# Optimization experiments

Hardware: AMD Instinct MI355X
Metric: run time of the kernel (lower is better)

## Reference

```python
import jax, jax.numpy as jnp
import numpy as np

EPS = 1e-5
N_HEADS = 16
D_NOPE = 128
D_ROPE = 64
D_QK = D_NOPE + D_ROPE  # 192
D_V = 128
KV_RANK = 512
SCALE = D_QK ** -0.5


def rms_norm(x, w, eps=EPS):
    return x * jax.lax.rsqrt(jnp.mean(x * x, axis=-1, keepdims=True) + eps) * w


def apply_rope(x, c, s):
    # x: [..., D_ROPE], c/s broadcastable [..., D_ROPE//2]; half-split rotation
    x0, x1 = x[..., : D_ROPE // 2], x[..., D_ROPE // 2 :]
    return jnp.concatenate([x0 * c - x1 * s, x0 * s + x1 * c], axis=-1)


def setup_inputs() -> dict:
    key = jax.random.key(0)
    ks = jax.random.split(key, 8)
    B, S, H_DIM = 2, 2048, 2048
    Q_RANK = 1536
    w = lambda k, shp: jax.random.normal(k, shp, dtype=jnp.float32) * 0.02
    # real RoPE tables: [max_seq, D_ROPE//2]
    inv_freq = 1.0 / (10000.0 ** (np.arange(0, D_ROPE, 2, dtype=np.float32) / D_ROPE))
    ang = np.arange(S, dtype=np.float32)[:, None] * inv_freq[None, :]
    return {
        "x": jax.random.normal(ks[0], (B, S, H_DIM), dtype=jnp.float32),
        "positions": jnp.arange(S, dtype=jnp.int64),
        "Wqa": w(ks[1], (H_DIM, Q_RANK)),
        "g_qa": jnp.ones((Q_RANK,), jnp.float32),
        "Wqb": w(ks[2], (Q_RANK, N_HEADS * D_QK)),
        "Wkva": w(ks[3], (H_DIM, KV_RANK + D_ROPE)),
        "g_kva": jnp.ones((KV_RANK,), jnp.float32),
        "Wkvb": w(ks[4], (KV_RANK, N_HEADS * (D_NOPE + D_V))),
        "Wo": w(ks[5], (N_HEADS * D_V, H_DIM)),
        "cos": jnp.asarray(np.cos(ang)),
        "sin": jnp.asarray(np.sin(ang)),
    }


def reference(x, positions, Wqa, g_qa, Wqb, Wkva, g_kva, Wkvb, Wo, cos, sin):
    B, S, _ = x.shape
    # Q path: low-rank down, RMSNorm, up
    q = rms_norm(x @ Wqa, g_qa) @ Wqb  # [B,S,H*D_QK]
    q = q.reshape(B, S, N_HEADS, D_QK)
    q_nope, q_rope = q[..., :D_NOPE], q[..., D_NOPE:]
    c = cos[positions]  # [S, D_ROPE//2]
    s = sin[positions]
    q_rope = apply_rope(q_rope, c[None, :, None, :], s[None, :, None, :])
    # KV path: joint down-proj, split latent / rope-key
    kv_a = x @ Wkva  # [B,S,KV_RANK+D_ROPE]
    kv_latent = rms_norm(kv_a[..., :KV_RANK], g_kva)
    k_rope = apply_rope(kv_a[..., KV_RANK:], c[None, :, :], s[None, :, :])  # [B,S,D_ROPE]
    # up-project latent to per-head k_nope and v
    kv_b = (kv_latent @ Wkvb).reshape(B, S, N_HEADS, D_NOPE + D_V)
    k_nope, v = kv_b[..., :D_NOPE], kv_b[..., D_NOPE:]
    k = jnp.concatenate(
        [k_nope, jnp.broadcast_to(k_rope[:, :, None, :], (B, S, N_HEADS, D_ROPE))], axis=-1
    )  # [B,S,H,D_QK]
    q_full = jnp.concatenate([q_nope, q_rope], axis=-1)  # [B,S,H,D_QK]
    # causal SDPA with d_qk != d_v
    scores = jnp.einsum("bqhd,bkhd->bhqk", q_full, k) * SCALE
    causal = jnp.tril(jnp.ones((S, S), dtype=bool))
    scores = jnp.where(causal[None, None, :, :], scores, -jnp.inf)
    p = jax.nn.softmax(scores, axis=-1)
    out = jnp.einsum("bhqk,bkhd->bqhd", p, v).reshape(B, S, N_HEADS * D_V)
    return out @ Wo
```

## Files before the change

kernel.cpp:

```cpp
#include <hip/hip_runtime.h>
#include <hip/hip_bf16.h>

typedef __bf16 bf16;
typedef __bf16 bf16x8 __attribute__((ext_vector_type(8)));
typedef __bf16 bf16x4 __attribute__((ext_vector_type(4)));
typedef float f32x4 __attribute__((ext_vector_type(4)));

#define B_    2
#define S_    2048
#define HD    2048
#define NH    16
#define DQK   192
#define DV    128
#define QR    1536
#define KVR   512
#define NTOK  4096
#define NKVB  4096
#define NQB   3072
#define NQKVA 2176

#define EXP2F(x) __builtin_amdgcn_exp2f(x)

static __device__ __forceinline__ void gload16(const void* g, void* l) {
  __builtin_amdgcn_global_load_lds(
      (const __attribute__((address_space(1))) void*)g,
      (__attribute__((address_space(3))) void*)l, 16, 0, 0);
}

__global__ __launch_bounds__(256) void cvt_bf16(const float* __restrict__ in,
                                                bf16* __restrict__ out, long n) {
  long i = ((long)blockIdx.x * 256 + threadIdx.x) * 4;
  if (i + 3 < n) {
    float4 v = *(const float4*)(in + i);
    bf16x4 o = {(bf16)v.x, (bf16)v.y, (bf16)v.z, (bf16)v.w};
    *(bf16x4*)(out + i) = o;
  }
}

__global__ __launch_bounds__(256) void transpose_cvt(const float* __restrict__ in,
                                                     bf16* __restrict__ out,
                                                     int R, int C, int Np) {
  __shared__ float tile[32][33];
  int c0 = blockIdx.x * 32;
  int r0 = blockIdx.y * 32;
  int tx = threadIdx.x & 31, ty = threadIdx.x >> 5;
#pragma unroll
  for (int i = 0; i < 4; ++i) {
    int r = r0 + ty + i * 8, c = c0 + tx;
    tile[ty + i * 8][tx] = (c < C) ? in[(long)r * C + c] : 0.f;
  }
  __syncthreads();
#pragma unroll
  for (int i = 0; i < 4; ++i) {
    int oc = c0 + ty + i * 8;
    if (oc < Np) out[(long)oc * R + r0 + tx] = (bf16)tile[tx][ty + i * 8];
  }
}

#define GEMM_CORE(A, Bt, K)                                                    \
  __shared__ bf16 As[128 * 64];                                                \
  __shared__ bf16 Bs[128 * 64];                                                \
  const int t = threadIdx.x;                                                   \
  const int l = t & 63;                                                        \
  const int w = t >> 6;                                                        \
  const int m0 = blockIdx.y * 128;                                             \
  const int n0 = blockIdx.x * 128;                                             \
  const int wr = (w >> 1) * 64;                                                \
  const int wc = (w & 1) * 64;                                                 \
  const int lr = l & 15;                                                       \
  const int lg = l >> 4;                                                       \
  f32x4 acc[4][4] = {};                                                        \
  for (int k0 = 0; k0 < (K); k0 += 64) {                                       \
    __syncthreads();                                                           \
    _Pragma("unroll")                                                          \
    for (int j = 0; j < 4; ++j) {                                              \
      int s = j * 256 + t;                                                     \
      int row = s >> 3, sc = s & 7;                                            \
      int c = sc ^ (row & 7);                                                  \
      gload16((A) + (long)(m0 + row) * (K) + k0 + c * 8,                       \
              As + (j * 256 + w * 64) * 8);                                    \
      gload16((Bt) + (long)(n0 + row) * (K) + k0 + c * 8,                      \
              Bs + (j * 256 + w * 64) * 8);                                    \
    }                                                                          \
    __syncthreads();                                                           \
    _Pragma("unroll")                                                          \
    for (int kh = 0; kh < 2; ++kh) {                                           \
      bf16x8 af[4], bfr[4];                                                    \
      _Pragma("unroll")                                                        \
      for (int m = 0; m < 4; ++m) {                                            \
        int row = wr + m * 16 + lr;                                            \
        af[m] = *(const bf16x8*)(As + row * 64 + (((kh * 4 + lg) ^ (row & 7)) << 3)); \
      }                                                                        \
      _Pragma("unroll")                                                        \
      for (int n = 0; n < 4; ++n) {                                            \
        int row = wc + n * 16 + lr;                                            \
        bfr[n] = *(const bf16x8*)(Bs + row * 64 + (((kh * 4 + lg) ^ (row & 7)) << 3)); \
      }                                                                        \
      _Pragma("unroll")                                                        \
      for (int m = 0; m < 4; ++m)                                              \
        _Pragma("unroll")                                                      \
        for (int n = 0; n < 4; ++n)                                            \
          acc[m][n] = __builtin_amdgcn_mfma_f32_16x16x32_bf16(af[m], bfr[n], acc[m][n], 0, 0, 0); \
    }                                                                          \
  }

template <typename CT>
__global__ __launch_bounds__(256) void gemm_bf16(const bf16* __restrict__ A,
                                                 const bf16* __restrict__ Bt,
                                                 CT* __restrict__ C,
                                                 int M, int N, int K) {
  GEMM_CORE(A, Bt, K)
#pragma unroll
  for (int m = 0; m < 4; ++m)
#pragma unroll
    for (int n = 0; n < 4; ++n)
#pragma unroll
      for (int v = 0; v < 4; ++v) {
        int row = m0 + wr + m * 16 + lg * 4 + v;
        int col = n0 + wc + n * 16 + lr;
        C[(long)row * N + col] = (CT)acc[m][n][v];
      }
}

__global__ __launch_bounds__(256) void gemm_qf(const bf16* __restrict__ A,
                                               const bf16* __restrict__ Bt,
                                               const int* __restrict__ pos,
                                               const float* __restrict__ cosT,
                                               const float* __restrict__ sinT,
                                               bf16* __restrict__ q_bhsd) {
  const float SCALE = 0.07216878364870323f * 1.4426950408889634f;
  GEMM_CORE(A, Bt, QR)
  int c0 = n0 + wc;
  int h = c0 / 192;
  int part = c0 - h * 192;
#pragma unroll
  for (int m = 0; m < 4; ++m)
#pragma unroll
    for (int v = 0; v < 4; ++v) {
      int row = m0 + wr + m * 16 + lg * 4 + v;
      int b = row >> 11, s = row & (S_ - 1);
      long base = ((long)(b * NH + h) * S_ + s) * DQK;
      if (part < 128) {
#pragma unroll
        for (int n = 0; n < 4; ++n)
          q_bhsd[base + part + n * 16 + lr] = (bf16)(acc[m][n][v] * SCALE);
      } else {
        int p = pos[s] & (S_ - 1);
        float c_lo = cosT[p * 32 + lr],      s_lo = sinT[p * 32 + lr];
        float c_hi = cosT[p * 32 + 16 + lr], s_hi = sinT[p * 32 + 16 + lr];
        float o0 = acc[m][0][v] * c_lo - acc[m][2][v] * s_lo;
        float o1 = acc[m][1][v] * c_hi - acc[m][3][v] * s_hi;
        float o2 = acc[m][0][v] * s_lo + acc[m][2][v] * c_lo;
        float o3 = acc[m][1][v] * s_hi + acc[m][3][v] * c_hi;
        q_bhsd[base + 128 + lr] = (bf16)(o0 * SCALE);
        q_bhsd[base + 144 + lr] = (bf16)(o1 * SCALE);
        q_bhsd[base + 160 + lr] = (bf16)(o2 * SCALE);
        q_bhsd[base + 176 + lr] = (bf16)(o3 * SCALE);
      }
    }
}

__global__ __launch_bounds__(256) void gemm_kvb(const bf16* __restrict__ A,
                                                const bf16* __restrict__ Bt,
                                                bf16* __restrict__ k_bhsd,
                                                bf16* __restrict__ v_rows) {
  GEMM_CORE(A, Bt, KVR)
  int c0 = n0 + wc;
  int h = c0 >> 8;
  int dbase = c0 & 64;
  bool vpart = (c0 >> 7) & 1;
#pragma unroll
  for (int m = 0; m < 4; ++m)
#pragma unroll
    for (int v = 0; v < 4; ++v) {
      int row = m0 + wr + m * 16 + lg * 4 + v;
      int b = row >> 11, s = row & (S_ - 1);
      if (!vpart) {
        long base = ((long)(b * NH + h) * S_ + s) * DQK + dbase;
#pragma unroll
        for (int n = 0; n < 4; ++n)
          k_bhsd[base + n * 16 + lr] = (bf16)acc[m][n][v];
      } else {
        long base = (long)row * 2048 + h * 128 + dbase;
#pragma unroll
        for (int n = 0; n < 4; ++n)
          v_rows[base + n * 16 + lr] = (bf16)acc[m][n][v];
      }
    }
}

__global__ __launch_bounds__(256) void norm_prep(const bf16* __restrict__ xa,
                                                 const float* __restrict__ g_qa,
                                                 const float* __restrict__ g_kva,
                                                 const int* __restrict__ pos,
                                                 const float* __restrict__ cosT,
                                                 const float* __restrict__ sinT,
                                                 bf16* __restrict__ q_n,
                                                 bf16* __restrict__ kv_l,
                                                 bf16* __restrict__ k_bhsd) {
  int row = blockIdx.x;
  int t = threadIdx.x;
  int b = row >> 11, s = row & (S_ - 1);
  const bf16* xr = xa + (long)row * NQKVA;
  __shared__ float red[3];
  __shared__ bf16 rope_s[64];
  float vf[8];
  if (t < 192) {
    bf16x8 vv = *(const bf16x8*)(xr + t * 8);
    float ss = 0.f;
#pragma unroll
    for (int e = 0; e < 8; ++e) { vf[e] = (float)vv[e]; ss += vf[e] * vf[e]; }
#pragma unroll
    for (int m = 1; m < 64; m <<= 1) ss += __shfl_xor(ss, m);
    if ((t & 63) == 0) red[t >> 6] = ss;
  } else {
    int tt = t - 192;
    const bf16* xl = xr + QR;
    bf16x8 vv = *(const bf16x8*)(xl + tt * 8);
    float ss = 0.f;
#pragma unroll
    for (int e = 0; e < 8; ++e) { vf[e] = (float)vv[e]; ss += vf[e] * vf[e]; }
#pragma unroll
    for (int m = 1; m < 64; m <<= 1) ss += __shfl_xor(ss, m);
    float rs = rsqrtf(ss / KVR + 1e-5f);
    bf16x8 o;
#pragma unroll
    for (int e = 0; e < 8; ++e) o[e] = (bf16)(vf[e] * rs * g_kva[tt * 8 + e]);
    *(bf16x8*)(kv_l + (long)row * KVR + tt * 8) = o;
    if (tt < 32) {
      int p = pos[s] & (S_ - 1);
      float c = cosT[p * 32 + tt], sn = sinT[p * 32 + tt];
      float x0 = (float)xl[512 + tt], x1 = (float)xl[544 + tt];
      rope_s[tt] = (bf16)(x0 * c - x1 * sn);
      rope_s[32 + tt] = (bf16)(x0 * sn + x1 * c);
    }
  }
  __syncthreads();
  if (t < 192) {
    float ss = red[0] + red[1] + red[2];
    float rs = rsqrtf(ss / QR + 1e-5f);
    bf16x8 o;
#pragma unroll
    for (int e = 0; e < 8; ++e) o[e] = (bf16)(vf[e] * rs * g_qa[t * 8 + e]);
    *(bf16x8*)(q_n + (long)row * QR + t * 8) = o;
  } else {
    int tt = t - 192;
    bf16x8 rv = *(const bf16x8*)&rope_s[(tt & 7) * 8];
    long base0 = ((long)(b * NH + (tt >> 3)) * S_ + s) * DQK + 128 + (tt & 7) * 8;
    long base1 = ((long)(b * NH + 8 + (tt >> 3)) * S_ + s) * DQK + 128 + (tt & 7) * 8;
    *(bf16x8*)(k_bhsd + base0) = rv;
    *(bf16x8*)(k_bhsd + base1) = rv;
  }
}

__global__ __launch_bounds__(256) void v_trans(const bf16* __restrict__ v_rows,
                                               bf16* __restrict__ v_t) {
  __shared__ bf16 tile[32][33];
  int st = blockIdx.x, dt = blockIdx.y, bh = blockIdx.z;
  int b = bh >> 4, h = bh & 15;
  int tx = threadIdx.x & 31, ty = threadIdx.x >> 5;
#pragma unroll
  for (int i = 0; i < 4; ++i) {
    int s = st * 32 + ty + i * 8, d = dt * 32 + tx;
    tile[ty + i * 8][tx] = v_rows[((long)(b * S_ + s)) * 2048 + h * 128 + d];
  }
  __syncthreads();
#pragma unroll
  for (int i = 0; i < 4; ++i) {
    int d = dt * 32 + ty + i * 8, s = st * 32 + tx;
    v_t[((long)bh * DV + d) * S_ + s] = tile[tx][ty + i * 8];
  }
}

#define QBLK 64
#define KVB  64
#define DVP  144
__global__ __launch_bounds__(256) void flash2(const bf16* __restrict__ q_bhsd,
                                              const bf16* __restrict__ k_bhsd,
                                              const bf16* __restrict__ v_t,
                                              bf16* __restrict__ att) {
  __shared__ bf16 Ks[KVB * DQK];
  __shared__ bf16 Vs[DVP * KVB];
  __shared__ bf16 Ps[4][16 * 72];
  int bid = blockIdx.x;
  int bh = bid & 31;
  int qt = 31 - (bid >> 5);
  int b = bh >> 4, h = bh & 15;
  int q0 = qt * QBLK;
  int t = threadIdx.x;
  int w = t >> 6, l = t & 63;
  int lr = l & 15, lg = l >> 4;
  int qw = q0 + w * 16;

  const bf16* Qb = q_bhsd + (long)bh * S_ * DQK;
  const bf16* Kb = k_bhsd + (long)bh * S_ * DQK;
  const bf16* Vb = v_t + (long)bh * DV * S_;

  if (t < 128) {
    int rr = 128 + (t >> 3), cc = (t & 7) * 8;
    bf16 val = (bf16)((rr == 128) ? 1.0f : 0.0f);
    bf16x8 vvv = {val, val, val, val, val, val, val, val};
    *(bf16x8*)(Vs + rr * KVB + cc) = vvv;
  }

  bf16x8 qf[6];
#pragma unroll
  for (int t6 = 0; t6 < 6; ++t6)
    qf[t6] = *(const bf16x8*)(Qb + (long)(qw + lr) * DQK + t6 * 32 + lg * 8);

  f32x4 oacc[9] = {};
  float mrow[4] = {-1e30f, -1e30f, -1e30f, -1e30f};
  const int lr7 = lr & 7;

  int nkt = qt + 1;
  for (int kt = 0; kt < nkt; ++kt) {
    int k0 = kt * KVB;
    __syncthreads();
#pragma unroll
    for (int j = 0; j < 6; ++j) {
      int s = j * 256 + t;
      int r = s / 24, c1 = s - r * 24;
      int c = c1 ^ (r & 7);
      gload16(Kb + (long)(k0 + r) * DQK + c * 8, Ks + (j * 256 + w * 64) * 8);
    }
#pragma unroll
    for (int j = 0; j < 4; ++j) {
      int s = j * 256 + t;
      int d = s >> 3, c1 = s & 7;
      int c = c1 ^ (d & 7);
      gload16(Vb + (long)d * S_ + k0 + c * 8, Vs + (j * 256 + w * 64) * 8);
    }
    __syncthreads();
    if (k0 > qw + 15) continue;

    f32x4 sacc[4] = {};
#pragma unroll
    for (int n = 0; n < 4; ++n) {
      int rk = n * 16 + lr;
#pragma unroll
      for (int t6 = 0; t6 < 6; ++t6) {
        bf16x8 kf = *(const bf16x8*)(Ks + rk * DQK + (((t6 * 4 + lg) ^ lr7) << 3));
        sacc[n] = __builtin_amdgcn_mfma_f32_16x16x32_bf16(qf[t6], kf, sacc[n], 0, 0, 0);
      }
    }
    if (k0 + KVB - 1 > qw) {
#pragma unroll
      for (int n = 0; n < 4; ++n)
#pragma unroll
        for (int v = 0; v < 4; ++v) {
          int r = lg * 4 + v, c = n * 16 + lr;
          if (k0 + c > qw + r) sacc[n][v] = -1e30f;
        }
    }
    float corr[4], p[4][4];
#pragma unroll
    for (int v = 0; v < 4; ++v) {
      float mv = fmaxf(fmaxf(sacc[0][v], sacc[1][v]), fmaxf(sacc[2][v], sacc[3][v]));
#pragma unroll
      for (int msk = 1; msk < 16; msk <<= 1) mv = fmaxf(mv, __shfl_xor(mv, msk));
      float mt = fmaxf(mrow[v], mv);
      corr[v] = EXP2F(mrow[v] - mt);
#pragma unroll
      for (int n = 0; n < 4; ++n) p[n][v] = EXP2F(sacc[n][v] - mt);
      mrow[v] = mt;
    }
#pragma unroll
    for (int dn = 0; dn < 9; ++dn)
#pragma unroll
      for (int v = 0; v < 4; ++v) oacc[dn][v] *= corr[v];
#pragma unroll
    for (int v = 0; v < 4; ++v)
#pragma unroll
      for (int n = 0; n < 4; ++n)
        Ps[w][(lg * 4 + v) * 72 + n * 16 + lr] = (bf16)p[n][v];
#pragma unroll
    for (int kc = 0; kc < 2; ++kc) {
      bf16x8 pf = *(const bf16x8*)(Ps[w] + lr * 72 + kc * 32 + lg * 8);
#pragma unroll
      for (int dn = 0; dn < 9; ++dn) {
        int d = dn * 16 + lr;
        bf16x8 vf = *(const bf16x8*)(Vs + d * KVB + (((kc * 4 + lg) ^ lr7) << 3));
        oacc[dn] = __builtin_amdgcn_mfma_f32_16x16x32_bf16(pf, vf, oacc[dn], 0, 0, 0);
      }
    }
  }
  float rl[4];
#pragma unroll
  for (int v = 0; v < 4; ++v) {
    float lv = __shfl(oacc[8][v], lg * 16);
    rl[v] = 1.0f / lv;
  }
#pragma unroll
  for (int dn = 0; dn < 8; ++dn)
#pragma unroll
    for (int v = 0; v < 4; ++v) {
      int r = lg * 4 + v;
      float o = oacc[dn][v] * rl[v];
      att[((long)(b * S_ + qw + r)) * 2048 + h * 128 + dn * 16 + lr] = (bf16)o;
    }
}

extern "C" void kernel_launch(void* const* d_in, const int* in_sizes, int n_in,
                              void* d_out, int out_size, void* d_ws, size_t ws_size,
                              hipStream_t stream) {
  const float* x        = (const float*)d_in[0];
  const int* pos        = (const int*)d_in[1];
  const float* Wqa      = (const float*)d_in[2];
  const float* g_qa     = (const float*)d_in[3];
  const float* Wqb      = (const float*)d_in[4];
  const float* Wkva     = (const float*)d_in[5];
  const float* g_kva    = (const float*)d_in[6];
  const float* Wkvb     = (const float*)d_in[7];
  const float* Wo       = (const float*)d_in[8];
  const float* cosT     = (const float*)d_in[9];
  const float* sinT     = (const float*)d_in[10];
  float* out            = (float*)d_out;

  size_t off = 0;
  char* wsp = (char*)d_ws;
  auto alloc = [&](size_t n) { void* p = wsp + off; off += (n + 255) & ~(size_t)255; return p; };
  bf16*  Wqa_t  = (bf16*) alloc((size_t)QR * HD * 2);
  bf16*  Wkva_t = (bf16*) alloc((size_t)640 * HD * 2);
  bf16*  Wqb_t  = (bf16*) alloc((size_t)NQB * QR * 2);
  bf16*  Wkvb_t = (bf16*) alloc((size_t)NKVB * KVR * 2);
  bf16*  Wo_t   = (bf16*) alloc((size_t)HD * HD * 2);
  bf16*  x_bf   = (bf16*) alloc((size_t)NTOK * HD * 2);
  bf16*  q_bhsd = (bf16*) alloc((size_t)B_ * NH * S_ * DQK * 2);
  bf16*  k_bhsd = (bf16*) alloc((size_t)B_ * NH * S_ * DQK * 2);
  bf16*  v_rows = (bf16*) alloc((size_t)NTOK * 2048 * 2);
  bf16*  v_t    = (bf16*) alloc((size_t)B_ * NH * DV * S_ * 2);
  bf16*  att    = (bf16*) alloc((size_t)NTOK * 2048 * 2);
  char*  T      = (char*) alloc((size_t)33554432);
  bf16*  xa  = (bf16*)T;
  bf16*  q_n = (bf16*)(T + 18874368);
  bf16*  kv_l = (bf16*)(T + 18874368 + 12582912);
  if (ws_size < off) return;

  cvt_bf16<<<(NTOK * HD / 4 + 255) / 256, 256, 0, stream>>>(x, x_bf, (long)NTOK * HD);
  transpose_cvt<<<dim3(QR / 32, HD / 32), 256, 0, stream>>>(Wqa, Wqa_t, HD, QR, QR);
  transpose_cvt<<<dim3(640 / 32, HD / 32), 256, 0, stream>>>(Wkva, Wkva_t, HD, 576, 640);
  transpose_cvt<<<dim3(NQB / 32, QR / 32), 256, 0, stream>>>(Wqb, Wqb_t, QR, NQB, NQB);
  transpose_cvt<<<dim3(NKVB / 32, KVR / 32), 256, 0, stream>>>(Wkvb, Wkvb_t, KVR, NKVB, NKVB);
  transpose_cvt<<<dim3(HD / 32, HD / 32), 256, 0, stream>>>(Wo, Wo_t, HD, HD, HD);
  gemm_bf16<bf16><<<dim3(NQKVA / 128, NTOK / 128), 256, 0, stream>>>(x_bf, Wqa_t, xa, NTOK, NQKVA, HD);
  norm_prep<<<NTOK, 256, 0, stream>>>(xa, g_qa, g_kva, pos, cosT, sinT, q_n, kv_l, k_bhsd);
  gemm_qf<<<dim3(NQB / 128, NTOK / 128), 256, 0, stream>>>(q_n, Wqb_t, pos, cosT, sinT, q_bhsd);
  gemm_kvb<<<dim3(NKVB / 128, NTOK / 128), 256, 0, stream>>>(kv_l, Wkvb_t, k_bhsd, v_rows);
  v_trans<<<dim3(S_ / 32, DV / 32, B_ * NH), 256, 0, stream>>>(v_rows, v_t);
  flash2<<<1024, 256, 0, stream>>>(q_bhsd, k_bhsd, v_t, att);
  gemm_bf16<float><<<dim3(HD / 128, NTOK / 128), 256, 0, stream>>>(att, Wo_t, out, NTOK, HD, HD);
}
```

Before: 334.8 us.

## Merge weight transposes into one launch and add lazy softmax rescaling

The five weight transpose-convert launches are replaced by a single kernel that picks its segment from the block index, which removes four launches and their tail gaps. Separately, the flash attention loop now rescales the running max and output accumulators only when some row's new max exceeds the stored max by more than a threshold of 8 (log2 domain), and skips the per-tile correction multiply otherwise. The exponentials are then taken against a possibly stale max, so values can grow up to 2^8 before rescaling. This relies on fp32 headroom and bf16 P values staying accurate.

```diff
diff --git a/kernel.cpp b/kernel.cpp
--- a/kernel.cpp
+++ b/kernel.cpp
@@ -37,12 +37,27 @@
   }
 }
 
-__global__ __launch_bounds__(256) void transpose_cvt(const float* __restrict__ in,
-                                                     bf16* __restrict__ out,
-                                                     int R, int C, int Np) {
+struct TransArgs {
+  const float *s0, *s1, *s2, *s3, *s4;
+  bf16 *d0, *d1, *d2, *d3, *d4;
+};
+__global__ __launch_bounds__(256) void transpose_all(TransArgs a) {
   __shared__ float tile[32][33];
-  int c0 = blockIdx.x * 32;
-  int r0 = blockIdx.y * 32;
+  int bid = blockIdx.x;
+  int seg, rel;
+  if      (bid < 3072)  { seg = 0; rel = bid; }
+  else if (bid < 4352)  { seg = 1; rel = bid - 3072; }
+  else if (bid < 8960)  { seg = 2; rel = bid - 4352; }
+  else if (bid < 11008) { seg = 3; rel = bid - 8960; }
+  else                  { seg = 4; rel = bid - 11008; }
+  const float* in = seg == 0 ? a.s0 : seg == 1 ? a.s1 : seg == 2 ? a.s2 : seg == 3 ? a.s3 : a.s4;
+  bf16* out       = seg == 0 ? a.d0 : seg == 1 ? a.d1 : seg == 2 ? a.d2 : seg == 3 ? a.d3 : a.d4;
+  int R   = seg == 0 ? 2048 : seg == 1 ? 2048 : seg == 2 ? 1536 : seg == 3 ? 512 : 2048;
+  int C   = seg == 0 ? 1536 : seg == 1 ? 576  : seg == 2 ? 3072 : seg == 3 ? 4096 : 2048;
+  int Np  = seg == 0 ? 1536 : seg == 1 ? 640  : seg == 2 ? 3072 : seg == 3 ? 4096 : 2048;
+  int nbx = seg == 0 ? 48   : seg == 1 ? 20   : seg == 2 ? 96   : seg == 3 ? 128 : 64;
+  int c0 = (rel % nbx) * 32;
+  int r0 = (rel / nbx) * 32;
   int tx = threadIdx.x & 31, ty = threadIdx.x >> 5;
 #pragma unroll
   for (int i = 0; i < 4; ++i) {
@@ -352,27 +367,33 @@
           if (k0 + c > qw + r) sacc[n][v] = -1e30f;
         }
     }
-    float corr[4], p[4][4];
+    float mv[4];
 #pragma unroll
     for (int v = 0; v < 4; ++v) {
-      float mv = fmaxf(fmaxf(sacc[0][v], sacc[1][v]), fmaxf(sacc[2][v], sacc[3][v]));
-#pragma unroll
-      for (int msk = 1; msk < 16; msk <<= 1) mv = fmaxf(mv, __shfl_xor(mv, msk));
-      float mt = fmaxf(mrow[v], mv);
-      corr[v] = EXP2F(mrow[v] - mt);
-#pragma unroll
-      for (int n = 0; n < 4; ++n) p[n][v] = EXP2F(sacc[n][v] - mt);
-      mrow[v] = mt;
-    }
-#pragma unroll
-    for (int dn = 0; dn < 9; ++dn)
-#pragma unroll
-      for (int v = 0; v < 4; ++v) oacc[dn][v] *= corr[v];
+      mv[v] = fmaxf(fmaxf(sacc[0][v], sacc[1][v]), fmaxf(sacc[2][v], sacc[3][v]));
+#pragma unroll
+      for (int msk = 1; msk < 16; msk <<= 1) mv[v] = fmaxf(mv[v], __shfl_xor(mv[v], msk));
+    }
+    bool grow = (mv[0] > mrow[0] + 8.f) | (mv[1] > mrow[1] + 8.f) |
+                (mv[2] > mrow[2] + 8.f) | (mv[3] > mrow[3] + 8.f);
+    if (__any(grow)) {
+      float corr[4];
+#pragma unroll
+      for (int v = 0; v < 4; ++v) {
+        float mt = fmaxf(mrow[v], mv[v]);
+        corr[v] = EXP2F(mrow[v] - mt);
+        mrow[v] = mt;
+      }
+#pragma unroll
+      for (int dn = 0; dn < 9; ++dn)
+#pragma unroll
+        for (int v = 0; v < 4; ++v) oacc[dn][v] *= corr[v];
+    }
 #pragma unroll
     for (int v = 0; v < 4; ++v)
 #pragma unroll
       for (int n = 0; n < 4; ++n)
-        Ps[w][(lg * 4 + v) * 72 + n * 16 + lr] = (bf16)p[n][v];
+        Ps[w][(lg * 4 + v) * 72 + n * 16 + lr] = (bf16)EXP2F(sacc[n][v] - mrow[v]);
 #pragma unroll
     for (int kc = 0; kc < 2; ++kc) {
       bf16x8 pf = *(const bf16x8*)(Ps[w] + lr * 72 + kc * 32 + lg * 8);
@@ -437,11 +458,8 @@
   if (ws_size < off) return;
 
   cvt_bf16<<<(NTOK * HD / 4 + 255) / 256, 256, 0, stream>>>(x, x_bf, (long)NTOK * HD);
-  transpose_cvt<<<dim3(QR / 32, HD / 32), 256, 0, stream>>>(Wqa, Wqa_t, HD, QR, QR);
-  transpose_cvt<<<dim3(640 / 32, HD / 32), 256, 0, stream>>>(Wkva, Wkva_t, HD, 576, 640);
-  transpose_cvt<<<dim3(NQB / 32, QR / 32), 256, 0, stream>>>(Wqb, Wqb_t, QR, NQB, NQB);
-  transpose_cvt<<<dim3(NKVB / 32, KVR / 32), 256, 0, stream>>>(Wkvb, Wkvb_t, KVR, NKVB, NKVB);
-  transpose_cvt<<<dim3(HD / 32, HD / 32), 256, 0, stream>>>(Wo, Wo_t, HD, HD, HD);
+  TransArgs ta = {Wqa, Wkva, Wqb, Wkvb, Wo, Wqa_t, Wkva_t, Wqb_t, Wkvb_t, Wo_t};
+  transpose_all<<<15104, 256, 0, stream>>>(ta);
   gemm_bf16<bf16><<<dim3(NQKVA / 128, NTOK / 128), 256, 0, stream>>>(x_bf, Wqa_t, xa, NTOK, NQKVA, HD);
   norm_prep<<<NTOK, 256, 0, stream>>>(xa, g_qa, g_kva, pos, cosT, sinT, q_n, kv_l, k_bhsd);
   gemm_qf<<<dim3(NQB / 128, NTOK / 128), 256, 0, stream>>>(q_n, Wqb_t, pos, cosT, sinT, q_bhsd);
```

Result: faster. 325.3 us (-2.8%).
